# Kernel optimization log

Hardware: AMD Instinct MI355X
Metric: run time of the kernel (lower is better)

The kernel has to match this reference:

```python
import jax, jax.numpy as jnp
import numpy as np

D = 256      # d_model
H = 8        # num heads
HD = D // H  # head dim
DFF = 1024   # feedforward dim
S = 1024     # seq len
B = 8        # batch
EPS = 1e-5


def _layernorm(x, g, b):
    mu = jnp.mean(x, axis=-1, keepdims=True)
    var = jnp.mean((x - mu) ** 2, axis=-1, keepdims=True)
    return (x - mu) * jax.lax.rsqrt(var + EPS) * g + b


def setup_inputs() -> dict:
    key = jax.random.key(0)
    ks = jax.random.split(key, 12)
    xav = lambda k, shape: jax.random.uniform(
        k, shape, jnp.float32, -1.0, 1.0) * np.sqrt(6.0 / (shape[0] + shape[-1]))
    return {
        "src": jax.random.normal(ks[0], (S, B, D), jnp.float32),
        "bias": jax.random.normal(ks[1], (B, H, S, S), jnp.float32),
        "in_proj_w": xav(ks[2], (3 * D, D)),
        "in_proj_b": jnp.zeros((3 * D,), jnp.float32),
        "out_w": xav(ks[3], (D, D)),
        "out_b": jnp.zeros((D,), jnp.float32),
        "w1": xav(ks[4], (DFF, D)),
        "b1": jnp.zeros((DFF,), jnp.float32),
        "w2": xav(ks[5], (D, DFF)),
        "b2": jnp.zeros((D,), jnp.float32),
        "g1": jnp.ones((D,), jnp.float32),
        "be1": jnp.zeros((D,), jnp.float32),
        "g2": jnp.ones((D,), jnp.float32),
        "be2": jnp.zeros((D,), jnp.float32),
    }


def reference(src, bias, in_proj_w, in_proj_b, out_w, out_b,
              w1, b1, w2, b2, g1, be1, g2, be2):
    # Pre-norm (note: residual uses the NORMED src, matching the torch code)
    x = _layernorm(src, g1, be1)                       # [S,B,D]
    qkv = x @ in_proj_w.T + in_proj_b                  # [S,B,3D]
    q, k, v = jnp.split(qkv, 3, axis=-1)
    q = q * (HD ** -0.5)
    # [S,B,D] -> [B,H,S,HD]
    to_heads = lambda t: t.reshape(S, B, H, HD).transpose(1, 2, 0, 3)
    qh, kh, vh = to_heads(q), to_heads(k), to_heads(v)
    scores = jnp.einsum('bhsd,bhtd->bhst', qh, kh) + bias
    attn = jax.nn.softmax(scores, axis=-1)             # [B,H,S,S]
    ctx = jnp.einsum('bhst,bhtd->bhsd', attn, vh)      # [B,H,S,HD]
    ctx = ctx.transpose(2, 0, 1, 3).reshape(S, B, D)
    attn_out = ctx @ out_w.T + out_b
    x = x + attn_out                                   # residual (eval: no dropout)
    y = _layernorm(x, g2, be2)
    ff = jax.nn.relu(y @ w1.T + b1) @ w2.T + b2
    return y + ff
```

## Files before the change

### kernel.cpp

```cpp
#include <hip/hip_runtime.h>
#include <hip/hip_bf16.h>
#include <cstdint>

typedef unsigned short u16;
typedef __attribute__((ext_vector_type(8))) short bf16x8;
typedef __attribute__((ext_vector_type(4))) float f32x4;

#define S_LEN 1024
#define BATCH 8
#define DMODEL 256
#define NHEAD 8
#define HDIM 32
#define DFF 1024
#define NROWS (S_LEN * BATCH)

static __device__ __forceinline__ u16 f2b(float f) {
    union { float f; unsigned u; } x{f};
    unsigned r = (x.u + 0x7fffu + ((x.u >> 16) & 1u)) >> 16;
    return (u16)r;
}
static __device__ __forceinline__ float b2f(unsigned h) {
    union { unsigned u; float f; } x{h << 16};
    return x.f;
}

__global__ __launch_bounds__(256) void prep_kernel(
    const float* __restrict__ in, const float* __restrict__ g1,
    const float* __restrict__ be1, u16* __restrict__ ob,
    const float* __restrict__ ipw, const float* __restrict__ outw,
    const float* __restrict__ w1, const float* __restrict__ w2,
    const float* __restrict__ ipb,
    u16* __restrict__ wqkv, u16* __restrict__ wout,
    u16* __restrict__ w1b, u16* __restrict__ w2b, float* __restrict__ bq)
{
    const float s = 0.17677669529663689f;
    if (blockIdx.x >= 2048) {
        const int i4 = ((int)blockIdx.x - 2048) * 1024 + threadIdx.x * 4;
        const float* src; u16* dst; int off; float sc = 1.0f;
        if (i4 < 196608)      { src = ipw;  dst = wqkv; off = 0;      if (i4 < 65536) sc = s; }
        else if (i4 < 262144) { src = outw; dst = wout; off = 196608; }
        else if (i4 < 524288) { src = w1;   dst = w1b;  off = 262144; }
        else                  { src = w2;   dst = w2b;  off = 524288; }
        const float4 v = *(const float4*)(src + i4 - off);
        uint2 pk;
        pk.x = (unsigned)f2b(v.x * sc) | ((unsigned)f2b(v.y * sc) << 16);
        pk.y = (unsigned)f2b(v.z * sc) | ((unsigned)f2b(v.w * sc) << 16);
        *(uint2*)(dst + i4 - off) = pk;
        if (i4 < 768) {
            const float4 b = *(const float4*)(ipb + i4);
            const float bs = (i4 < 256) ? s : 1.0f;
            *(float4*)(bq + i4) = make_float4(b.x * bs, b.y * bs, b.z * bs, b.w * bs);
        }
        return;
    }
    const int w = threadIdx.x >> 6, l = threadIdx.x & 63;
    const int row = blockIdx.x * 4 + w;
    const float4 v = *(const float4*)(in + (size_t)row * DMODEL + l * 4);
    float s0 = v.x + v.y + v.z + v.w;
    #pragma unroll
    for (int o = 32; o; o >>= 1) s0 += __shfl_xor(s0, o);
    const float mu = s0 * (1.0f / DMODEL);
    const float dx = v.x - mu, dy = v.y - mu, dz = v.z - mu, dw = v.w - mu;
    float sq = dx * dx + dy * dy + dz * dz + dw * dw;
    #pragma unroll
    for (int o = 32; o; o >>= 1) sq += __shfl_xor(sq, o);
    const float rs = rsqrtf(sq * (1.0f / DMODEL) + 1e-5f);
    const float4 gv = *(const float4*)(g1 + l * 4);
    const float4 bv = *(const float4*)(be1 + l * 4);
    const float r0 = dx * rs * gv.x + bv.x;
    const float r1 = dy * rs * gv.y + bv.y;
    const float r2 = dz * rs * gv.z + bv.z;
    const float r3 = dw * rs * gv.w + bv.w;
    uint2 pk;
    pk.x = (unsigned)f2b(r0) | ((unsigned)f2b(r1) << 16);
    pk.y = (unsigned)f2b(r2) | ((unsigned)f2b(r3) << 16);
    *(uint2*)(ob + (size_t)row * DMODEL + l * 4) = pk;
}

template <int MF, int NF>
__device__ __forceinline__ void gemm_core(
    const u16* __restrict__ A, const u16* __restrict__ Bw,
    int K, int nbase, int rowbase, u16* sB, f32x4 acc[MF][NF])
{
    const int tid = threadIdx.x, w = tid >> 6, l = tid & 63;
    const int g = l >> 4, q = l & 15;
    const u16* Arow = A + (size_t)(rowbase + w * (MF * 16) + q) * K + g * 8;

    const int sbr = tid >> 3, sseg = tid & 7;
    const int LOADS = NF / 2;
    const int CHUNK = NF * 16 * 128;
    size_t bsrc[LOADS];
    int d[LOADS];
    #pragma unroll
    for (int i = 0; i < LOADS; ++i) {
        bsrc[i] = (size_t)(nbase + sbr + 32 * i) * K + sseg * 8;
        d[i] = (sbr + 32 * i) * 128 + ((sseg * 16) ^ ((sbr & 7) << 4));
    }

    {
        #pragma unroll
        for (int i = 0; i < LOADS; ++i) {
            const uint4 r = *(const uint4*)(Bw + bsrc[i]);
            *(uint4*)((char*)sB + d[i]) = r;
        }
    }
    const int NC = K >> 6;
    for (int c = 0; c < NC; ++c) {
        __syncthreads();
        char* sBc = (char*)sB + (c & 1) * CHUNK;
        char* sBn = (char*)sB + ((c + 1) & 1) * CHUNK;
        uint4 p[LOADS];
        if (c + 1 < NC) {
            #pragma unroll
            for (int i = 0; i < LOADS; ++i)
                p[i] = *(const uint4*)(Bw + bsrc[i] + (c + 1) * 64);
        }
        const int kk = c * 64;
        #pragma unroll
        for (int ks = 0; ks < 2; ++ks) {
            bf16x8 af[MF];
            #pragma unroll
            for (int m = 0; m < MF; ++m)
                af[m] = *(const bf16x8*)(Arow + (size_t)m * 16 * K + kk + ks * 32);
            #pragma unroll
            for (int n = 0; n < NF; ++n) {
                const int rr = n * 16 + q;
                const bf16x8 bf = *(const bf16x8*)(
                    sBc + rr * 128 + ((ks * 64 + g * 16) ^ ((rr & 7) << 4)));
                #pragma unroll
                for (int m = 0; m < MF; ++m)
                    acc[m][n] = __builtin_amdgcn_mfma_f32_16x16x32_bf16(bf, af[m], acc[m][n], 0, 0, 0);
            }
        }
        if (c + 1 < NC) {
            #pragma unroll
            for (int i = 0; i < LOADS; ++i)
                *(uint4*)(sBn + d[i]) = p[i];
        }
    }
}

__global__ __launch_bounds__(256) void gemm_qkv(
    const u16* __restrict__ A, const u16* __restrict__ Bw,
    const float* __restrict__ bias,
    u16* __restrict__ Qh, u16* __restrict__ Kh, u16* __restrict__ Vt)
{
    __shared__ u16 sB[2][128 * 64];
    const int tid = threadIdx.x, w = tid >> 6, l = tid & 63;
    const int g = l >> 4, q = l & 15;
    const int rowbase = blockIdx.x * 128, nbase = blockIdx.y * 128;
    f32x4 acc[2][8] = {};
    gemm_core<2, 8>(A, Bw, 256, nbase, rowbase, &sB[0][0], acc);

    #pragma unroll
    for (int m = 0; m < 2; ++m) {
        const int row = rowbase + w * 32 + m * 16 + q;
        const int s = row >> 3, b = row & 7;
        #pragma unroll
        for (int n = 0; n < 8; ++n) {
            const int col = nbase + n * 16 + g * 4;
            const float4 bv = *(const float4*)(bias + col);
            if (col < 512) {
                u16* dst = (col >= 256) ? Kh : Qh;
                const int cc = col & 255, h = cc >> 5, hd = cc & 31;
                const int bh = b * 8 + h;
                uint2 pk;
                pk.x = (unsigned)f2b(acc[m][n][0] + bv.x) | ((unsigned)f2b(acc[m][n][1] + bv.y) << 16);
                pk.y = (unsigned)f2b(acc[m][n][2] + bv.z) | ((unsigned)f2b(acc[m][n][3] + bv.w) << 16);
                *(uint2*)(dst + ((size_t)bh * S_LEN + s) * HDIM + hd) = pk;
            } else {
                const int cc = col - 512, h = cc >> 5, hd = cc & 31;
                const int bh = b * 8 + h;
                Vt[((size_t)bh * HDIM + hd + 0) * S_LEN + s] = f2b(acc[m][n][0] + bv.x);
                Vt[((size_t)bh * HDIM + hd + 1) * S_LEN + s] = f2b(acc[m][n][1] + bv.y);
                Vt[((size_t)bh * HDIM + hd + 2) * S_LEN + s] = f2b(acc[m][n][2] + bv.z);
                Vt[((size_t)bh * HDIM + hd + 3) * S_LEN + s] = f2b(acc[m][n][3] + bv.w);
            }
        }
    }
}

__global__ __launch_bounds__(256) void gemm_ffn1(
    const u16* __restrict__ A, const u16* __restrict__ Bw,
    const float* __restrict__ bias, u16* __restrict__ outb)
{
    __shared__ u16 sB[2][128 * 64];
    const int tid = threadIdx.x, w = tid >> 6, l = tid & 63;
    const int g = l >> 4, q = l & 15;
    const int rowbase = blockIdx.x * 128, nbase = blockIdx.y * 128;
    f32x4 acc[2][8] = {};
    gemm_core<2, 8>(A, Bw, 256, nbase, rowbase, &sB[0][0], acc);

    #pragma unroll
    for (int m = 0; m < 2; ++m) {
        const int row = rowbase + w * 32 + m * 16 + q;
        #pragma unroll
        for (int n = 0; n < 8; ++n) {
            const int col = nbase + n * 16 + g * 4;
            const float4 bv = *(const float4*)(bias + col);
            const float v0 = fmaxf(acc[m][n][0] + bv.x, 0.f);
            const float v1 = fmaxf(acc[m][n][1] + bv.y, 0.f);
            const float v2 = fmaxf(acc[m][n][2] + bv.z, 0.f);
            const float v3 = fmaxf(acc[m][n][3] + bv.w, 0.f);
            uint2 pk;
            pk.x = (unsigned)f2b(v0) | ((unsigned)f2b(v1) << 16);
            pk.y = (unsigned)f2b(v2) | ((unsigned)f2b(v3) << 16);
            *(uint2*)(outb + (size_t)row * DFF + col) = pk;
        }
    }
}

__global__ __launch_bounds__(256) void gemm_ffn2(
    const u16* __restrict__ A, const u16* __restrict__ Bw,
    const float* __restrict__ bias, const u16* __restrict__ resid,
    float* __restrict__ outf)
{
    __shared__ u16 sB[2][64 * 64];
    const int tid = threadIdx.x, w = tid >> 6, l = tid & 63;
    const int g = l >> 4, q = l & 15;
    const int rowbase = blockIdx.x * 128, nbase = blockIdx.y * 64;
    f32x4 acc[2][4] = {};
    gemm_core<2, 4>(A, Bw, 1024, nbase, rowbase, &sB[0][0], acc);

    #pragma unroll
    for (int m = 0; m < 2; ++m) {
        const int row = rowbase + w * 32 + m * 16 + q;
        #pragma unroll
        for (int n = 0; n < 4; ++n) {
            const int col = nbase + n * 16 + g * 4;
            const float4 bv = *(const float4*)(bias + col);
            const uint2 rp = *(const uint2*)(resid + (size_t)row * DMODEL + col);
            *(float4*)(outf + (size_t)row * DMODEL + col) = make_float4(
                acc[m][n][0] + bv.x + b2f(rp.x & 0xffffu),
                acc[m][n][1] + bv.y + b2f(rp.x >> 16),
                acc[m][n][2] + bv.z + b2f(rp.y & 0xffffu),
                acc[m][n][3] + bv.w + b2f(rp.y >> 16));
        }
    }
}

__global__ __launch_bounds__(256) void attn_kernel(
    const u16* __restrict__ Qh, const u16* __restrict__ Kh,
    const u16* __restrict__ Vt, const float* __restrict__ bias,
    u16* __restrict__ ctx)
{
    __shared__ u16 sK[2][64 * 32];
    __shared__ u16 sV[2][32 * 64];
    __shared__ u16 sP[4][16 * 64];
    const int tid = threadIdx.x, w = tid >> 6, l = tid & 63;
    const int g = l >> 4, q = l & 15;
    const int bh = blockIdx.x, b = bh >> 3, h = bh & 7;
    const int qbase = blockIdx.y * 64 + w * 16;
    const int qrow = qbase + q;

    const bf16x8 qf = *(const bf16x8*)(Qh + ((size_t)bh * S_LEN + qrow) * HDIM + g * 8);
    const float* brow = bias + ((size_t)bh * S_LEN + qrow) * S_LEN;
    u16* Pw = sP[w];
    const int swz = (q & 7) << 4;

    const u16* KsrcBase = Kh + ((size_t)bh * S_LEN + w * 16 + q) * HDIM + g * 8;
    const u16* VsrcBase = Vt + ((size_t)bh * HDIM + (w & 1) * 16 + q) * S_LEN
                             + (w >> 1) * 32 + g * 8;
    u16* KdstA = &sK[0][tid * 8]; u16* KdstB = &sK[1][tid * 8];
    u16* VdstA = &sV[0][tid * 8]; u16* VdstB = &sV[1][tid * 8];

    f32x4 ctxa[2] = {{0,0,0,0},{0,0,0,0}};
    float m = -1e30f, lsum = 0.f;

    auto loadB = [&](int kt, f32x4* bv) {
        #pragma unroll
        for (int n = 0; n < 4; ++n)
            bv[n] = __builtin_nontemporal_load(
                (const f32x4*)(brow + kt * 64 + n * 16 + g * 4));
    };

    auto proc = [&](int buf, const f32x4* bv) {
        f32x4 sc[4];
        #pragma unroll
        for (int n = 0; n < 4; ++n) {
            const bf16x8 kf = *(const bf16x8*)(&sK[buf][(n * 64 + l) * 8]);
            f32x4 z = {0, 0, 0, 0};
            sc[n] = __builtin_amdgcn_mfma_f32_16x16x32_bf16(kf, qf, z, 0, 0, 0);
        }
        #pragma unroll
        for (int n = 0; n < 4; ++n)
            #pragma unroll
            for (int r = 0; r < 4; ++r) sc[n][r] += bv[n][r];

        float mx = sc[0][0];
        #pragma unroll
        for (int n = 0; n < 4; ++n)
            #pragma unroll
            for (int r = 0; r < 4; ++r) mx = fmaxf(mx, sc[n][r]);
        mx = fmaxf(mx, __shfl_xor(mx, 16));
        mx = fmaxf(mx, __shfl_xor(mx, 32));
        const float mn = fmaxf(m, mx);
        const float corr = __expf(m - mn);
        float su = 0.f;
        u16 pb[16];
        #pragma unroll
        for (int n = 0; n < 4; ++n)
            #pragma unroll
            for (int r = 0; r < 4; ++r) {
                const float pv = __expf(sc[n][r] - mn);
                su += pv;
                pb[n * 4 + r] = f2b(pv);
            }
        su += __shfl_xor(su, 16);
        su += __shfl_xor(su, 32);
        lsum = lsum * corr + su;
        m = mn;
        #pragma unroll
        for (int jg = 0; jg < 2; ++jg)
            #pragma unroll
            for (int r = 0; r < 4; ++r) ctxa[jg][r] *= corr;

        #pragma unroll
        for (int n = 0; n < 4; ++n) {
            uint2 pk;
            pk.x = (unsigned)pb[n * 4] | ((unsigned)pb[n * 4 + 1] << 16);
            pk.y = (unsigned)pb[n * 4 + 2] | ((unsigned)pb[n * 4 + 3] << 16);
            *(uint2*)((char*)Pw + q * 128 + ((n * 32 + g * 8) ^ swz)) = pk;
        }

        #pragma unroll
        for (int ks = 0; ks < 2; ++ks) {
            const bf16x8 pf = *(const bf16x8*)((char*)Pw + q * 128 + ((ks * 64 + g * 16) ^ swz));
            #pragma unroll
            for (int jg = 0; jg < 2; ++jg) {
                const bf16x8 vf = *(const bf16x8*)(&sV[buf][((ks * 2 + jg) * 64 + l) * 8]);
                ctxa[jg] = __builtin_amdgcn_mfma_f32_16x16x32_bf16(vf, pf, ctxa[jg], 0, 0, 0);
            }
        }
    };

    f32x4 bv0[4], bv1[4];
    {
        const uint4 kr = *(const uint4*)(KsrcBase);
        const uint4 vr = *(const uint4*)(VsrcBase);
        *(uint4*)KdstA = kr;
        *(uint4*)VdstA = vr;
        loadB(0, bv0);
    }
    __syncthreads();

    for (int kt = 0; kt < 16; kt += 2) {
        {
            uint4 kr, vr;
            kr = *(const uint4*)(KsrcBase + (size_t)(kt + 1) * 64 * HDIM);
            vr = *(const uint4*)(VsrcBase + (size_t)(kt + 1) * 64);
            loadB(kt + 1, bv1);
            proc(0, bv0);
            *(uint4*)KdstB = kr;
            *(uint4*)VdstB = vr;
        }
        __syncthreads();
        {
            uint4 kr, vr;
            if (kt + 2 < 16) {
                kr = *(const uint4*)(KsrcBase + (size_t)(kt + 2) * 64 * HDIM);
                vr = *(const uint4*)(VsrcBase + (size_t)(kt + 2) * 64);
                loadB(kt + 2, bv0);
            }
            proc(1, bv1);
            if (kt + 2 < 16) {
                *(uint4*)KdstA = kr;
                *(uint4*)VdstA = vr;
            }
        }
        __syncthreads();
    }

    const float inv = 1.0f / lsum;
    #pragma unroll
    for (int jg = 0; jg < 2; ++jg) {
        uint2 pk;
        pk.x = (unsigned)f2b(ctxa[jg][0] * inv) | ((unsigned)f2b(ctxa[jg][1] * inv) << 16);
        pk.y = (unsigned)f2b(ctxa[jg][2] * inv) | ((unsigned)f2b(ctxa[jg][3] * inv) << 16);
        *(uint2*)(ctx + ((size_t)qrow * 8 + b) * DMODEL + h * 32 + jg * 16 + g * 4) = pk;
    }
}

__global__ __launch_bounds__(256) void oproj_ln(
    const u16* __restrict__ ctx, const u16* __restrict__ wob,
    const float* __restrict__ ob, const u16* __restrict__ xb,
    const float* __restrict__ g2, const float* __restrict__ be2,
    u16* __restrict__ yb)
{
    __shared__ float s1[4][32], s2[4][32];
    const int tid = threadIdx.x, wv = tid >> 6, l = tid & 63;
    const int g = l >> 4, q = l & 15;
    const int rowbase = blockIdx.x * 32;
    f32x4 acc[2][4] = {};
    const u16* Arow = ctx + (size_t)(rowbase + q) * 256 + g * 8;
    const u16* Brow = wob + (size_t)(wv * 64 + q) * 256 + g * 8;

    #pragma unroll 2
    for (int kk = 0; kk < 256; kk += 32) {
        bf16x8 af[2];
        #pragma unroll
        for (int m = 0; m < 2; ++m)
            af[m] = *(const bf16x8*)(Arow + (size_t)m * 16 * 256 + kk);
        #pragma unroll
        for (int n = 0; n < 4; ++n) {
            const bf16x8 bf = *(const bf16x8*)(Brow + (size_t)n * 16 * 256 + kk);
            #pragma unroll
            for (int m = 0; m < 2; ++m)
                acc[m][n] = __builtin_amdgcn_mfma_f32_16x16x32_bf16(bf, af[m], acc[m][n], 0, 0, 0);
        }
    }

    float sum[2] = {0.f, 0.f};
    #pragma unroll
    for (int m = 0; m < 2; ++m) {
        const int row = rowbase + m * 16 + q;
        #pragma unroll
        for (int n = 0; n < 4; ++n) {
            const int col = wv * 64 + n * 16 + g * 4;
            const float4 bv = *(const float4*)(ob + col);
            const uint2 rp = *(const uint2*)(xb + (size_t)row * 256 + col);
            acc[m][n][0] += bv.x + b2f(rp.x & 0xffffu);
            acc[m][n][1] += bv.y + b2f(rp.x >> 16);
            acc[m][n][2] += bv.z + b2f(rp.y & 0xffffu);
            acc[m][n][3] += bv.w + b2f(rp.y >> 16);
            sum[m] += acc[m][n][0] + acc[m][n][1] + acc[m][n][2] + acc[m][n][3];
        }
        sum[m] += __shfl_xor(sum[m], 16);
        sum[m] += __shfl_xor(sum[m], 32);
    }
    if (l < 16) { s1[wv][q] = sum[0]; s1[wv][16 + q] = sum[1]; }
    __syncthreads();
    float mu[2], rs[2];
    #pragma unroll
    for (int m = 0; m < 2; ++m) {
        const int lr = m * 16 + q;
        mu[m] = (s1[0][lr] + s1[1][lr] + s1[2][lr] + s1[3][lr]) * (1.0f / 256);
    }
    float sq[2] = {0.f, 0.f};
    #pragma unroll
    for (int m = 0; m < 2; ++m) {
        #pragma unroll
        for (int n = 0; n < 4; ++n)
            #pragma unroll
            for (int r = 0; r < 4; ++r) {
                const float d = acc[m][n][r] - mu[m];
                sq[m] += d * d;
            }
        sq[m] += __shfl_xor(sq[m], 16);
        sq[m] += __shfl_xor(sq[m], 32);
    }
    if (l < 16) { s2[wv][q] = sq[0]; s2[wv][16 + q] = sq[1]; }
    __syncthreads();
    #pragma unroll
    for (int m = 0; m < 2; ++m) {
        const int lr = m * 16 + q;
        rs[m] = rsqrtf((s2[0][lr] + s2[1][lr] + s2[2][lr] + s2[3][lr]) * (1.0f / 256) + 1e-5f);
    }

    #pragma unroll
    for (int m = 0; m < 2; ++m) {
        const int row = rowbase + m * 16 + q;
        #pragma unroll
        for (int n = 0; n < 4; ++n) {
            const int col = wv * 64 + n * 16 + g * 4;
            const float4 gv = *(const float4*)(g2 + col);
            const float4 b2 = *(const float4*)(be2 + col);
            const float y0 = (acc[m][n][0] - mu[m]) * rs[m] * gv.x + b2.x;
            const float y1 = (acc[m][n][1] - mu[m]) * rs[m] * gv.y + b2.y;
            const float y2 = (acc[m][n][2] - mu[m]) * rs[m] * gv.z + b2.z;
            const float y3 = (acc[m][n][3] - mu[m]) * rs[m] * gv.w + b2.w;
            uint2 pk;
            pk.x = (unsigned)f2b(y0) | ((unsigned)f2b(y1) << 16);
            pk.y = (unsigned)f2b(y2) | ((unsigned)f2b(y3) << 16);
            *(uint2*)(yb + (size_t)row * 256 + col) = pk;
        }
    }
}

extern "C" void kernel_launch(void* const* d_in, const int* in_sizes, int n_in,
                              void* d_out, int out_size, void* d_ws, size_t ws_size,
                              hipStream_t stream)
{
    const float* src  = (const float*)d_in[0];
    const float* bias = (const float*)d_in[1];
    const float* ipw  = (const float*)d_in[2];
    const float* ipb  = (const float*)d_in[3];
    const float* outw = (const float*)d_in[4];
    const float* outb = (const float*)d_in[5];
    const float* w1   = (const float*)d_in[6];
    const float* b1   = (const float*)d_in[7];
    const float* w2   = (const float*)d_in[8];
    const float* b2   = (const float*)d_in[9];
    const float* g1   = (const float*)d_in[10];
    const float* be1  = (const float*)d_in[11];
    const float* g2   = (const float*)d_in[12];
    const float* be2  = (const float*)d_in[13];

    char* p = (char*)d_ws;
    auto alloc = [&](size_t bytes) -> void* {
        void* r = (void*)p;
        p += (bytes + 255) & ~(size_t)255;
        return r;
    };
    u16*   xb   = (u16*)  alloc((size_t)NROWS * DMODEL * 2);
    u16*   Qh   = (u16*)  alloc((size_t)64 * S_LEN * HDIM * 2);
    u16*   Kb   = (u16*)  alloc((size_t)64 * S_LEN * HDIM * 2);
    u16*   Vt   = (u16*)  alloc((size_t)64 * S_LEN * HDIM * 2);
    u16*   ctx  = (u16*)  alloc((size_t)NROWS * DMODEL * 2);
    u16*   yb   = (u16*)  alloc((size_t)NROWS * DMODEL * 2);
    u16*   hb   = (u16*)  alloc((size_t)NROWS * DFF * 2);
    u16*   wqkv = (u16*)  alloc((size_t)768 * 256 * 2);
    u16*   wob  = (u16*)  alloc((size_t)256 * 256 * 2);
    u16*   w1b  = (u16*)  alloc((size_t)1024 * 256 * 2);
    u16*   w2b  = (u16*)  alloc((size_t)256 * 1024 * 2);
    float* bq   = (float*)alloc(768 * 4);

    prep_kernel<<<2816, 256, 0, stream>>>(src, g1, be1, xb,
                                          ipw, outw, w1, w2, ipb,
                                          wqkv, wob, w1b, w2b, bq);
    gemm_qkv<<<dim3(64, 6), 256, 0, stream>>>(xb, wqkv, bq, Qh, Kb, Vt);
    attn_kernel<<<dim3(64, 16), 256, 0, stream>>>(Qh, Kb, Vt, bias, ctx);
    oproj_ln<<<256, 256, 0, stream>>>(ctx, wob, outb, xb, g2, be2, yb);
    gemm_ffn1<<<dim3(64, 8), 256, 0, stream>>>(yb, w1b, b1, hb);
    gemm_ffn2<<<dim3(64, 4), 256, 0, stream>>>(hb, w2b, b2, yb, (float*)d_out);
}
```

Measured before the change: 152.5 us.

## Use hardware bf16 pack, setprio around MFMAs, and widen grids for oproj/ffn2

```diff
diff --git a/kernel.cpp b/kernel.cpp
--- a/kernel.cpp
+++ b/kernel.cpp
@@ -22,6 +22,11 @@
 static __device__ __forceinline__ float b2f(unsigned h) {
     union { unsigned u; float f; } x{h << 16};
     return x.f;
+}
+static __device__ __forceinline__ unsigned cvtpk(float lo, float hi) {
+    unsigned r;
+    asm("v_cvt_pk_bf16_f32 %0, %1, %2" : "=v"(r) : "v"(lo), "v"(hi));
+    return r;
 }
 
 __global__ __launch_bounds__(256) void prep_kernel(
@@ -215,18 +220,18 @@
     const float* __restrict__ bias, const u16* __restrict__ resid,
     float* __restrict__ outf)
 {
-    __shared__ u16 sB[2][64 * 64];
+    __shared__ u16 sB[2][32 * 64];
     const int tid = threadIdx.x, w = tid >> 6, l = tid & 63;
     const int g = l >> 4, q = l & 15;
-    const int rowbase = blockIdx.x * 128, nbase = blockIdx.y * 64;
-    f32x4 acc[2][4] = {};
-    gemm_core<2, 4>(A, Bw, 1024, nbase, rowbase, &sB[0][0], acc);
+    const int rowbase = blockIdx.x * 128, nbase = blockIdx.y * 32;
+    f32x4 acc[2][2] = {};
+    gemm_core<2, 2>(A, Bw, 1024, nbase, rowbase, &sB[0][0], acc);
 
     #pragma unroll
     for (int m = 0; m < 2; ++m) {
         const int row = rowbase + w * 32 + m * 16 + q;
         #pragma unroll
-        for (int n = 0; n < 4; ++n) {
+        for (int n = 0; n < 2; ++n) {
             const int col = nbase + n * 16 + g * 4;
             const float4 bv = *(const float4*)(bias + col);
             const uint2 rp = *(const uint2*)(resid + (size_t)row * DMODEL + col);
@@ -276,36 +281,40 @@
 
     auto proc = [&](int buf, const f32x4* bv) {
         f32x4 sc[4];
+        __builtin_amdgcn_s_setprio(1);
         #pragma unroll
         for (int n = 0; n < 4; ++n) {
             const bf16x8 kf = *(const bf16x8*)(&sK[buf][(n * 64 + l) * 8]);
             f32x4 z = {0, 0, 0, 0};
             sc[n] = __builtin_amdgcn_mfma_f32_16x16x32_bf16(kf, qf, z, 0, 0, 0);
         }
+        __builtin_amdgcn_s_setprio(0);
         #pragma unroll
         for (int n = 0; n < 4; ++n)
             #pragma unroll
             for (int r = 0; r < 4; ++r) sc[n][r] += bv[n][r];
 
-        float mx = sc[0][0];
+        float mxn[4];
         #pragma unroll
         for (int n = 0; n < 4; ++n)
-            #pragma unroll
-            for (int r = 0; r < 4; ++r) mx = fmaxf(mx, sc[n][r]);
+            mxn[n] = fmaxf(fmaxf(sc[n][0], sc[n][1]), fmaxf(sc[n][2], sc[n][3]));
+        float mx = fmaxf(fmaxf(mxn[0], mxn[1]), fmaxf(mxn[2], mxn[3]));
         mx = fmaxf(mx, __shfl_xor(mx, 16));
         mx = fmaxf(mx, __shfl_xor(mx, 32));
         const float mn = fmaxf(m, mx);
         const float corr = __expf(m - mn);
-        float su = 0.f;
-        u16 pb[16];
-        #pragma unroll
-        for (int n = 0; n < 4; ++n)
-            #pragma unroll
-            for (int r = 0; r < 4; ++r) {
-                const float pv = __expf(sc[n][r] - mn);
-                su += pv;
-                pb[n * 4 + r] = f2b(pv);
-            }
+
+        float sun[4];
+        unsigned pkw[8];
+        #pragma unroll
+        for (int n = 0; n < 4; ++n) {
+            const float p0 = __expf(sc[n][0] - mn), p1 = __expf(sc[n][1] - mn);
+            const float p2 = __expf(sc[n][2] - mn), p3 = __expf(sc[n][3] - mn);
+            sun[n] = (p0 + p1) + (p2 + p3);
+            pkw[n * 2]     = cvtpk(p0, p1);
+            pkw[n * 2 + 1] = cvtpk(p2, p3);
+        }
+        float su = (sun[0] + sun[1]) + (sun[2] + sun[3]);
         su += __shfl_xor(su, 16);
         su += __shfl_xor(su, 32);
         lsum = lsum * corr + su;
@@ -318,19 +327,21 @@
         #pragma unroll
         for (int n = 0; n < 4; ++n) {
             uint2 pk;
-            pk.x = (unsigned)pb[n * 4] | ((unsigned)pb[n * 4 + 1] << 16);
-            pk.y = (unsigned)pb[n * 4 + 2] | ((unsigned)pb[n * 4 + 3] << 16);
+            pk.x = pkw[n * 2];
+            pk.y = pkw[n * 2 + 1];
             *(uint2*)((char*)Pw + q * 128 + ((n * 32 + g * 8) ^ swz)) = pk;
         }
 
         #pragma unroll
         for (int ks = 0; ks < 2; ++ks) {
             const bf16x8 pf = *(const bf16x8*)((char*)Pw + q * 128 + ((ks * 64 + g * 16) ^ swz));
+            __builtin_amdgcn_s_setprio(1);
             #pragma unroll
             for (int jg = 0; jg < 2; ++jg) {
                 const bf16x8 vf = *(const bf16x8*)(&sV[buf][((ks * 2 + jg) * 64 + l) * 8]);
                 ctxa[jg] = __builtin_amdgcn_mfma_f32_16x16x32_bf16(vf, pf, ctxa[jg], 0, 0, 0);
             }
+            __builtin_amdgcn_s_setprio(0);
         }
     };
 
@@ -375,25 +386,25 @@
     #pragma unroll
     for (int jg = 0; jg < 2; ++jg) {
         uint2 pk;
-        pk.x = (unsigned)f2b(ctxa[jg][0] * inv) | ((unsigned)f2b(ctxa[jg][1] * inv) << 16);
-        pk.y = (unsigned)f2b(ctxa[jg][2] * inv) | ((unsigned)f2b(ctxa[jg][3] * inv) << 16);
+        pk.x = cvtpk(ctxa[jg][0] * inv, ctxa[jg][1] * inv);
+        pk.y = cvtpk(ctxa[jg][2] * inv, ctxa[jg][3] * inv);
         *(uint2*)(ctx + ((size_t)qrow * 8 + b) * DMODEL + h * 32 + jg * 16 + g * 4) = pk;
     }
 }
 
-__global__ __launch_bounds__(256) void oproj_ln(
+__global__ __launch_bounds__(512) void oproj_ln(
     const u16* __restrict__ ctx, const u16* __restrict__ wob,
     const float* __restrict__ ob, const u16* __restrict__ xb,
     const float* __restrict__ g2, const float* __restrict__ be2,
     u16* __restrict__ yb)
 {
-    __shared__ float s1[4][32], s2[4][32];
+    __shared__ float s1[8][32], s2[8][32];
     const int tid = threadIdx.x, wv = tid >> 6, l = tid & 63;
     const int g = l >> 4, q = l & 15;
     const int rowbase = blockIdx.x * 32;
-    f32x4 acc[2][4] = {};
+    f32x4 acc[2][2] = {};
     const u16* Arow = ctx + (size_t)(rowbase + q) * 256 + g * 8;
-    const u16* Brow = wob + (size_t)(wv * 64 + q) * 256 + g * 8;
+    const u16* Brow = wob + (size_t)(wv * 32 + q) * 256 + g * 8;
 
     #pragma unroll 2
     for (int kk = 0; kk < 256; kk += 32) {
@@ -402,7 +413,7 @@
         for (int m = 0; m < 2; ++m)
             af[m] = *(const bf16x8*)(Arow + (size_t)m * 16 * 256 + kk);
         #pragma unroll
-        for (int n = 0; n < 4; ++n) {
+        for (int n = 0; n < 2; ++n) {
             const bf16x8 bf = *(const bf16x8*)(Brow + (size_t)n * 16 * 256 + kk);
             #pragma unroll
             for (int m = 0; m < 2; ++m)
@@ -415,8 +426,8 @@
     for (int m = 0; m < 2; ++m) {
         const int row = rowbase + m * 16 + q;
         #pragma unroll
-        for (int n = 0; n < 4; ++n) {
-            const int col = wv * 64 + n * 16 + g * 4;
+        for (int n = 0; n < 2; ++n) {
+            const int col = wv * 32 + n * 16 + g * 4;
             const float4 bv = *(const float4*)(ob + col);
             const uint2 rp = *(const uint2*)(xb + (size_t)row * 256 + col);
             acc[m][n][0] += bv.x + b2f(rp.x & 0xffffu);
@@ -434,13 +445,16 @@
     #pragma unroll
     for (int m = 0; m < 2; ++m) {
         const int lr = m * 16 + q;
-        mu[m] = (s1[0][lr] + s1[1][lr] + s1[2][lr] + s1[3][lr]) * (1.0f / 256);
+        float t = 0.f;
+        #pragma unroll
+        for (int i = 0; i < 8; ++i) t += s1[i][lr];
+        mu[m] = t * (1.0f / 256);
     }
     float sq[2] = {0.f, 0.f};
     #pragma unroll
     for (int m = 0; m < 2; ++m) {
         #pragma unroll
-        for (int n = 0; n < 4; ++n)
+        for (int n = 0; n < 2; ++n)
             #pragma unroll
             for (int r = 0; r < 4; ++r) {
                 const float d = acc[m][n][r] - mu[m];
@@ -454,15 +468,18 @@
     #pragma unroll
     for (int m = 0; m < 2; ++m) {
         const int lr = m * 16 + q;
-        rs[m] = rsqrtf((s2[0][lr] + s2[1][lr] + s2[2][lr] + s2[3][lr]) * (1.0f / 256) + 1e-5f);
+        float t = 0.f;
+        #pragma unroll
+        for (int i = 0; i < 8; ++i) t += s2[i][lr];
+        rs[m] = rsqrtf(t * (1.0f / 256) + 1e-5f);
     }
 
     #pragma unroll
     for (int m = 0; m < 2; ++m) {
         const int row = rowbase + m * 16 + q;
         #pragma unroll
-        for (int n = 0; n < 4; ++n) {
-            const int col = wv * 64 + n * 16 + g * 4;
+        for (int n = 0; n < 2; ++n) {
+            const int col = wv * 32 + n * 16 + g * 4;
             const float4 gv = *(const float4*)(g2 + col);
             const float4 b2 = *(const float4*)(be2 + col);
             const float y0 = (acc[m][n][0] - mu[m]) * rs[m] * gv.x + b2.x;
@@ -520,7 +537,7 @@
                                           wqkv, wob, w1b, w2b, bq);
     gemm_qkv<<<dim3(64, 6), 256, 0, stream>>>(xb, wqkv, bq, Qh, Kb, Vt);
     attn_kernel<<<dim3(64, 16), 256, 0, stream>>>(Qh, Kb, Vt, bias, ctx);
-    oproj_ln<<<256, 256, 0, stream>>>(ctx, wob, outb, xb, g2, be2, yb);
+    oproj_ln<<<256, 512, 0, stream>>>(ctx, wob, outb, xb, g2, be2, yb);
     gemm_ffn1<<<dim3(64, 8), 256, 0, stream>>>(yb, w1b, b1, hb);
-    gemm_ffn2<<<dim3(64, 4), 256, 0, stream>>>(hb, w2b, b2, yb, (float*)d_out);
-}
+    gemm_ffn2<<<dim3(64, 8), 256, 0, stream>>>(hb, w2b, b2, yb, (float*)d_out);
+}
```

Result: slower. 160.2 us (+5.1%).
